# Kernel tuning notes

Hardware: AMD Instinct MI355X
Metric: run time of the kernel (lower is better)

Reference implementation:

```python
import jax, jax.numpy as jnp
import numpy as np

NUM_HEADS = 16
HIDDEN = 64  # per-head dim


def setup_inputs() -> dict:
    key = jax.random.key(0)
    ks = jax.random.split(key, 7)
    B, Nq, S, D = 2, 2048, 2048, 1024
    return {
        "queries": jax.random.normal(ks[0], (B, Nq, D), jnp.float32),
        "keys": jax.random.normal(ks[1], (B, S, D), jnp.float32),
        "values": jax.random.normal(ks[2], (B, S, D), jnp.float32),
        "Wq": jax.random.normal(ks[3], (D, NUM_HEADS * HIDDEN), jnp.float32) * 0.02,
        "Wk": jax.random.normal(ks[4], (D, NUM_HEADS * HIDDEN), jnp.float32) * 0.02,
        "Wv": jax.random.normal(ks[5], (D, NUM_HEADS * HIDDEN), jnp.float32) * 0.02,
        "Wo": jax.random.normal(ks[6], (NUM_HEADS * HIDDEN, 1024), jnp.float32) * 0.02,
    }


def reference(queries, keys, values, Wq, Wk, Wv, Wo):
    B, Nq, _ = queries.shape
    S = keys.shape[1]
    H, dh = NUM_HEADS, HIDDEN
    # projections, split heads: [B, len, H, dh] -> [B, H, len, dh]
    Q = (queries @ Wq).reshape(B, Nq, H, dh).transpose(0, 2, 1, 3)
    K = (keys @ Wk).reshape(B, S, H, dh).transpose(0, 2, 1, 3)
    V = (values @ Wv).reshape(B, S, H, dh).transpose(0, 2, 1, 3)
    scores = jnp.einsum("bhqd,bhkd->bhqk", Q, K) / jnp.sqrt(jnp.float32(dh))
    # NOTE: faithful to original -- softmax over ALL keys, THEN multiply by
    # strictly-lower-triangular mask (triangular * (1 - diagonal)); no renorm.
    P = jax.nn.softmax(scores, axis=-1)
    mask = jnp.tril(jnp.ones((Nq, S), jnp.float32), -1)  # strict lower triangle
    Sout = jnp.einsum("bhqk,bhkd->bhqd", P * mask, V)
    merged = Sout.transpose(0, 2, 1, 3).reshape(B, Nq, H * dh)
    return merged @ Wo
```

## Files before the change

kernel.cpp:

```cpp
#include <hip/hip_runtime.h>
#include <hip/hip_bf16.h>
#include <stdint.h>


typedef __bf16 bf16x8 __attribute__((ext_vector_type(8)));
typedef float f32x4 __attribute__((ext_vector_type(4)));
typedef unsigned int u32x4 __attribute__((ext_vector_type(4)));

typedef const __attribute__((address_space(1))) void* gas_t;
typedef __attribute__((address_space(3))) void* las_t;

__device__ __forceinline__ unsigned short f2bf(float f) {
    unsigned int u = __float_as_uint(f);
    return (unsigned short)((u + 0x7FFFu + ((u >> 16) & 1u)) >> 16);
}

__device__ __forceinline__ float exp2_hw(float x) {
    float r;
    asm("v_exp_f32 %0, %1" : "=v"(r) : "v"(x));
    return r;
}

__global__ __launch_bounds__(256) void cast_qkv(
    const float* __restrict__ q, const float* __restrict__ k, const float* __restrict__ v,
    unsigned short* __restrict__ oq, unsigned short* __restrict__ ok, unsigned short* __restrict__ ov)
{
    const float* src = (blockIdx.z == 0) ? q : (blockIdx.z == 1) ? k : v;
    unsigned short* dst = (blockIdx.z == 0) ? oq : (blockIdx.z == 1) ? ok : ov;
    unsigned int i = blockIdx.x * 256u + threadIdx.x;
    float4 f = reinterpret_cast<const float4*>(src)[i];
    ushort4 o;
    o.x = f2bf(f.x); o.y = f2bf(f.y); o.z = f2bf(f.z); o.w = f2bf(f.w);
    reinterpret_cast<ushort4*>(dst)[i] = o;
}

__global__ __launch_bounds__(256) void transpose_w(
    const float* __restrict__ w0, const float* __restrict__ w1,
    const float* __restrict__ w2, const float* __restrict__ w3,
    unsigned short* __restrict__ t0, unsigned short* __restrict__ t1,
    unsigned short* __restrict__ t2, unsigned short* __restrict__ t3)
{
    const float* W = (blockIdx.z == 0) ? w0 : (blockIdx.z == 1) ? w1 : (blockIdx.z == 2) ? w2 : w3;
    unsigned short* T = (blockIdx.z == 0) ? t0 : (blockIdx.z == 1) ? t1 : (blockIdx.z == 2) ? t2 : t3;
    __shared__ float s[32][33];
    const int tx = threadIdx.x, ty = threadIdx.y;
    const int x = blockIdx.x * 32 + tx;
#pragma unroll
    for (int j = 0; j < 4; ++j)
        s[ty + 8 * j][tx] = W[(size_t)(blockIdx.y * 32 + ty + 8 * j) * 1024 + x];
    __syncthreads();
    const int xo = blockIdx.y * 32 + tx;
#pragma unroll
    for (int j = 0; j < 4; ++j)
        T[(size_t)(blockIdx.x * 32 + ty + 8 * j) * 1024 + xo] = f2bf(s[tx][ty + 8 * j]);
}

__global__ __launch_bounds__(256) void transpose_v(
    const unsigned short* __restrict__ Vp, unsigned short* __restrict__ Vt)
{
    __shared__ unsigned short s[64][68];
    const int tid = threadIdx.x;
    const int s0 = blockIdx.x * 64, h = blockIdx.y, b = blockIdx.z;
    const size_t inbase = ((size_t)(b * 2048 + s0)) * 1024 + h * 64;
#pragma unroll
    for (int r = 0; r < 4; ++r) {
        int idx = r * 256 + tid;
        int row = idx >> 4;
        int c4 = (idx & 15) * 4;
        ushort4 v = *(const ushort4*)(Vp + inbase + (size_t)row * 1024 + c4);
        *(ushort4*)&s[row][c4] = v;
    }
    __syncthreads();
    const size_t outbase = ((size_t)((b * 16 + h) * 64)) * 2048 + s0;
#pragma unroll
    for (int r = 0; r < 4; ++r) {
        int idx = r * 256 + tid;
        int drow = idx >> 4;
        int sc = (idx & 15) * 4;
        ushort4 v;
        v.x = s[sc][drow]; v.y = s[sc + 1][drow]; v.z = s[sc + 2][drow]; v.w = s[sc + 3][drow];
        *(ushort4*)(Vt + outbase + (size_t)drow * 2048 + sc) = v;
    }
}

template <int BM, int BN, int MODE>
__global__ __launch_bounds__(256) void gemm_bt(
    const unsigned short* __restrict__ A0, const unsigned short* __restrict__ A1,
    const unsigned short* __restrict__ A2,
    const unsigned short* __restrict__ B0, const unsigned short* __restrict__ B1,
    const unsigned short* __restrict__ B2,
    unsigned short* __restrict__ C0, unsigned short* __restrict__ C1,
    unsigned short* __restrict__ C2, float* __restrict__ Cf)
{
    constexpr int K = 1024;
    constexpr int WM = BM / 2, WN = BN / 2, MI = WM / 16, NI = WN / 16;
    __shared__ __align__(16) unsigned char lds[(BM + BN) * 64];
    unsigned char* lA = lds;
    unsigned char* lB = lds + BM * 64;

    const int tid = threadIdx.x;
    const int z = blockIdx.z;
    const unsigned short* A  = (MODE == 1 || z == 0) ? A0 : (z == 1) ? A1 : A2;
    const unsigned short* Bt = (MODE == 1 || z == 0) ? B0 : (z == 1) ? B1 : B2;
    const int m0 = blockIdx.y * BM, n0 = blockIdx.x * BN;
    const int w = tid >> 6, lane = tid & 63, g = lane >> 4, l15 = lane & 15;
    const int wr = w >> 1, wc = w & 1;

    f32x4 acc[MI][NI] = {};

    for (int k0 = 0; k0 < K; k0 += 32) {
#pragma unroll
        for (int r = 0; r < (BM * 64) / 4096; ++r) {
            const int o = (r * 256 + tid) * 16;
            const unsigned char* gp = (const unsigned char*)A
                + ((size_t)(m0 + (o >> 6)) * K + k0) * 2 + (o & 63);
            __builtin_amdgcn_global_load_lds((gas_t)gp,
                (las_t)(lA + (r * 256 + (tid & ~63)) * 16), 16, 0, 0);
        }
#pragma unroll
        for (int r = 0; r < (BN * 64) / 4096; ++r) {
            const int o = (r * 256 + tid) * 16;
            const unsigned char* gp = (const unsigned char*)Bt
                + ((size_t)(n0 + (o >> 6)) * K + k0) * 2 + (o & 63);
            __builtin_amdgcn_global_load_lds((gas_t)gp,
                (las_t)(lB + (r * 256 + (tid & ~63)) * 16), 16, 0, 0);
        }
        __syncthreads();

        bf16x8 a[MI], bfr[NI];
#pragma unroll
        for (int mi = 0; mi < MI; ++mi)
            a[mi] = *(const bf16x8*)(lA + (wr * WM + mi * 16 + l15) * 64 + g * 16);
#pragma unroll
        for (int ni = 0; ni < NI; ++ni)
            bfr[ni] = *(const bf16x8*)(lB + (wc * WN + ni * 16 + l15) * 64 + g * 16);
#pragma unroll
        for (int mi = 0; mi < MI; ++mi)
#pragma unroll
            for (int ni = 0; ni < NI; ++ni)
                acc[mi][ni] = __builtin_amdgcn_mfma_f32_16x16x32_bf16(a[mi], bfr[ni], acc[mi][ni], 0, 0, 0);
        __syncthreads();
    }

    if (MODE == 1) {
#pragma unroll
        for (int mi = 0; mi < MI; ++mi)
#pragma unroll
            for (int ni = 0; ni < NI; ++ni)
#pragma unroll
                for (int i = 0; i < 4; ++i) {
                    const int row = m0 + wr * WM + mi * 16 + 4 * g + i;
                    const int col = n0 + wc * WN + ni * 16 + l15;
                    Cf[(size_t)row * 1024 + col] = acc[mi][ni][i];
                }
    } else {
        unsigned short* C = (z == 0) ? C0 : (z == 1) ? C1 : C2;
        const float qscale = (z == 0) ? 0.18033688f : 1.0f;
#pragma unroll
        for (int mi = 0; mi < MI; ++mi)
#pragma unroll
            for (int ni = 0; ni < NI; ++ni)
#pragma unroll
                for (int i = 0; i < 4; ++i) {
                    const int row = m0 + wr * WM + mi * 16 + 4 * g + i;
                    const int col = n0 + wc * WN + ni * 16 + l15;
                    C[(size_t)row * 1024 + col] = f2bf(acc[mi][ni][i] * qscale);
                }
    }
}

__device__ __forceinline__ f32x4 qk_exp(const unsigned char* base, int rowoff,
                                        int ni, int g, int l15,
                                        bf16x8 aq0, bf16x8 aq1)
{
    const int row = rowoff + ni * 16 + l15;
    const int sw = (row & 7) << 4;
    const bf16x8 bk0 = *(const bf16x8*)(base + ((row * 128 + g * 16) ^ sw));
    const bf16x8 bk1 = *(const bf16x8*)(base + ((row * 128 + 64 + g * 16) ^ sw));
    f32x4 t = {};
    t = __builtin_amdgcn_mfma_f32_16x16x32_bf16(bk0, aq0, t, 0, 0, 0);
    t = __builtin_amdgcn_mfma_f32_16x16x32_bf16(bk1, aq1, t, 0, 0, 0);
    f32x4 r;
#pragma unroll
    for (int i = 0; i < 4; ++i) r[i] = exp2_hw(t[i]);
    return r;
}

__global__ __launch_bounds__(256) void attn_kernel(
    const unsigned short* __restrict__ Qp, const unsigned short* __restrict__ Kp,
    const unsigned short* __restrict__ Vt, unsigned short* __restrict__ mrg)
{
    __shared__ __align__(16) unsigned char lds[24576];
    __shared__ float dden[4][16];
    unsigned char* Ks = lds;
    unsigned char* Vs = lds + 8192;
    unsigned char* Ps = lds + 16384;

    const int tid = threadIdx.x;
    const int w = tid >> 6, lane = tid & 63, g = lane >> 4, l15 = lane & 15;
    const int bid = blockIdx.x;
    const int bh = (bid & 7) * 4 + ((bid >> 3) & 3);
    const int qt = 31 - (bid >> 5);
    const int b = bh >> 4, hd = bh & 15;
    const int q0 = qt * 64;

    bf16x8 aq0, aq1;
    {
        const unsigned short* qp = Qp + ((size_t)(b * 2048 + q0 + 16 * w + l15) * 1024 + hd * 64 + g * 8);
        aq0 = *(const bf16x8*)qp;
        aq1 = *(const bf16x8*)(qp + 32);
    }

    const unsigned char* Kbase = (const unsigned char*)Kp + ((size_t)(b * 2048) * 1024 + hd * 64) * 2;
    const unsigned char* Vbase = (const unsigned char*)Vt + ((size_t)bh * 64) * 2048 * 2;

    const int o0 = tid * 16,         r0 = o0 >> 7;
    const int o1 = (256 + tid) * 16, r1 = o1 >> 7;
    const int o2 = (512 + tid) * 16, r2 = o2 >> 7;
    const int o3 = (768 + tid) * 16, r3 = o3 >> 7;

    f32x4 oacc[4] = {};
    f32x4 dsum = {0.f, 0.f, 0.f, 0.f};

    const int prow = 16 * w + l15;
    const int pb   = prow * 128;
    const int psw  = l15 << 3;

    uint4 kr0, kr1, vr0, vr1, cr0, cr1, cr2, cr3;
    kr0 = *(const uint4*)(Kbase + (size_t)r0 * 2048 + (o0 & 127));
    kr1 = *(const uint4*)(Kbase + (size_t)r1 * 2048 + (o1 & 127));
    vr0 = *(const uint4*)(Vbase + (size_t)r0 * 4096 + (o0 & 127));
    vr1 = *(const uint4*)(Vbase + (size_t)r1 * 4096 + (o1 & 127));

    for (int t = 0; t <= qt; ++t) {
        __syncthreads();
        *(uint4*)(Ks + (o0 ^ ((r0 & 7) << 4))) = kr0;
        *(uint4*)(Ks + (o1 ^ ((r1 & 7) << 4))) = kr1;
        *(uint4*)(Vs + (o0 ^ ((r0 & 7) << 4))) = vr0;
        *(uint4*)(Vs + (o1 ^ ((r1 & 7) << 4))) = vr1;
        if (t < qt) {
            const int k1 = (t + 1) * 64;
            kr0 = *(const uint4*)(Kbase + (size_t)(k1 + r0) * 2048 + (o0 & 127));
            kr1 = *(const uint4*)(Kbase + (size_t)(k1 + r1) * 2048 + (o1 & 127));
            vr0 = *(const uint4*)(Vbase + (size_t)r0 * 4096 + (size_t)k1 * 2 + (o0 & 127));
            vr1 = *(const uint4*)(Vbase + (size_t)r1 * 4096 + (size_t)k1 * 2 + (o1 & 127));
        } else if (qt < 31) {
            const int kc = (qt + 1) * 64;
            const int nk = 2048 - kc;
            cr0 = *(const uint4*)(Kbase + (size_t)(kc + r0) * 2048 + (o0 & 127));
            cr1 = *(const uint4*)(Kbase + (size_t)(kc + r1) * 2048 + (o1 & 127));
            if (nk > 64) {
                cr2 = *(const uint4*)(Kbase + (size_t)(kc + r2) * 2048 + (o2 & 127));
                cr3 = *(const uint4*)(Kbase + (size_t)(kc + r3) * 2048 + (o3 & 127));
            }
        }
        __syncthreads();

        f32x4 pe[4];
#pragma unroll
        for (int ni = 0; ni < 4; ++ni) {
            pe[ni] = qk_exp(Ks, 0, ni, g, l15, aq0, aq1);
            dsum += pe[ni];
        }
        if (t == qt) {
#pragma unroll
            for (int ni = 0; ni < 4; ++ni)
#pragma unroll
                for (int i = 0; i < 4; ++i)
                    if (ni * 16 + 4 * g + i >= prow) pe[ni][i] = 0.f;
        }
#pragma unroll
        for (int ni = 0; ni < 4; ++ni) {
            unsigned int lo, hi;
            asm("v_cvt_pk_bf16_f32 %0, %1, %2" : "=v"(lo) : "v"(pe[ni][0]), "v"(pe[ni][1]));
            asm("v_cvt_pk_bf16_f32 %0, %1, %2" : "=v"(hi) : "v"(pe[ni][2]), "v"(pe[ni][3]));
            uint2 pv; pv.x = lo; pv.y = hi;
            *(uint2*)(Ps + ((pb + ni * 32 + g * 8) ^ psw)) = pv;
        }
#pragma unroll
        for (int kk = 0; kk < 2; ++kk) {
            const uint2 a0 = *(const uint2*)(Ps + ((pb + kk * 64 + g * 16) ^ psw));
            const uint2 a1 = *(const uint2*)(Ps + ((pb + kk * 64 + g * 16 + 8) ^ psw));
            u32x4 au; au.x = a0.x; au.y = a0.y; au.z = a1.x; au.w = a1.y;
            const bf16x8 pa = *(const bf16x8*)&au;
#pragma unroll
            for (int ni = 0; ni < 4; ++ni) {
                const int rv = ni * 16 + l15;
                const bf16x8 bv = *(const bf16x8*)(Vs + ((rv * 128 + kk * 64 + g * 16) ^ ((rv & 7) << 4)));
                oacc[ni] = __builtin_amdgcn_mfma_f32_16x16x32_bf16(pa, bv, oacc[ni], 0, 0, 0);
            }
        }
    }

    for (int kc = (qt + 1) * 64; kc < 2048; kc += 128) {
        const int nk = min(128, 2048 - kc);
        __syncthreads();
        *(uint4*)(lds + (o0 ^ ((r0 & 7) << 4))) = cr0;
        *(uint4*)(lds + (o1 ^ ((r1 & 7) << 4))) = cr1;
        if (nk > 64) {
            *(uint4*)(lds + (o2 ^ ((r2 & 7) << 4))) = cr2;
            *(uint4*)(lds + (o3 ^ ((r3 & 7) << 4))) = cr3;
        }
        const int kn = kc + 128;
        if (kn < 2048) {
            const int nk2 = 2048 - kn;
            cr0 = *(const uint4*)(Kbase + (size_t)(kn + r0) * 2048 + (o0 & 127));
            cr1 = *(const uint4*)(Kbase + (size_t)(kn + r1) * 2048 + (o1 & 127));
            if (nk2 > 64) {
                cr2 = *(const uint4*)(Kbase + (size_t)(kn + r2) * 2048 + (o2 & 127));
                cr3 = *(const uint4*)(Kbase + (size_t)(kn + r3) * 2048 + (o3 & 127));
            }
        }
        __syncthreads();
        for (int koff = 0; koff < nk; koff += 64)
#pragma unroll
            for (int ni = 0; ni < 4; ++ni)
                dsum += qk_exp(lds, koff, ni, g, l15, aq0, aq1);
    }

    float den = dsum[0] + dsum[1] + dsum[2] + dsum[3];
    den += __shfl_xor(den, 16, 64);
    den += __shfl_xor(den, 32, 64);
    if (lane < 16) dden[w][lane] = den;
    float inv[4];
#pragma unroll
    for (int i = 0; i < 4; ++i) inv[i] = 1.0f / dden[w][4 * g + i];
#pragma unroll
    for (int ni = 0; ni < 4; ++ni)
#pragma unroll
        for (int i = 0; i < 4; ++i) {
            const int row = q0 + 16 * w + 4 * g + i;
            mrg[((size_t)b * 2048 + row) * 1024 + hd * 64 + ni * 16 + l15] =
                f2bf(oacc[ni][i] * inv[i]);
        }
}

extern "C" void kernel_launch(void* const* d_in, const int* in_sizes, int n_in,
                              void* d_out, int out_size, void* d_ws, size_t ws_size,
                              hipStream_t stream)
{
    const float* q  = (const float*)d_in[0];
    const float* k  = (const float*)d_in[1];
    const float* v  = (const float*)d_in[2];
    const float* Wq = (const float*)d_in[3];
    const float* Wk = (const float*)d_in[4];
    const float* Wv = (const float*)d_in[5];
    const float* Wo = (const float*)d_in[6];
    float* out = (float*)d_out;

    unsigned short* ws = (unsigned short*)d_ws;
    const size_t TEN = (size_t)2 * 2048 * 1024;
    unsigned short* qbf = ws;
    unsigned short* kbf = ws + TEN;
    unsigned short* vbf = ws + 2 * TEN;
    unsigned short* Wqt = ws + 3 * TEN;
    unsigned short* Wkt = Wqt + 1024 * 1024;
    unsigned short* Wvt = Wkt + 1024 * 1024;
    unsigned short* Wot = Wvt + 1024 * 1024;
    unsigned short* Qp  = ws + 4 * TEN;
    unsigned short* Kp  = ws + 5 * TEN;
    unsigned short* Vp  = ws + 6 * TEN;
    unsigned short* Vt  = qbf;
    unsigned short* mrg = kbf;

    cast_qkv<<<dim3(4096, 1, 3), 256, 0, stream>>>(q, k, v, qbf, kbf, vbf);
    transpose_w<<<dim3(32, 32, 4), dim3(32, 8), 0, stream>>>(Wq, Wk, Wv, Wo, Wqt, Wkt, Wvt, Wot);
    gemm_bt<128, 128, 0><<<dim3(8, 32, 3), 256, 0, stream>>>(
        qbf, kbf, vbf, Wqt, Wkt, Wvt, Qp, Kp, Vp, nullptr);
    transpose_v<<<dim3(32, 16, 2), 256, 0, stream>>>(Vp, Vt);
    attn_kernel<<<dim3(1024, 1, 1), 256, 0, stream>>>(Qp, Kp, Vt, mrg);
    gemm_bt<64, 128, 1><<<dim3(8, 64, 1), 256, 0, stream>>>(
        mrg, nullptr, nullptr, Wot, nullptr, nullptr, nullptr, nullptr, nullptr, out);
}
```

Measured before the change: 228.3 us.

## Double-buffer K/V tiles in LDS and merge denominator loop into main loop

Replaces the two-phase loop (masked PV tiles, then a separate denominator-only pass over the remaining keys in 128-row chunks) with a single 32-iteration loop over 64-key tiles. K and V tiles are ping-ponged between two LDS buffers, which removes one __syncthreads per iteration. Tiles past the diagonal only compute exp sums and skip the V load and PV MFMAs. The trade-off is more LDS (about 40KB instead of 24KB), which may lower occupancy, and more barriers in the tail phase, since it now walks 64-key tiles instead of 128.

```diff
diff --git a/kernel.cpp b/kernel.cpp
--- a/kernel.cpp
+++ b/kernel.cpp
@@ -169,11 +169,11 @@
     }
 }
 
-__device__ __forceinline__ f32x4 qk_exp(const unsigned char* base, int rowoff,
+__device__ __forceinline__ f32x4 qk_exp(const unsigned char* base,
                                         int ni, int g, int l15,
                                         bf16x8 aq0, bf16x8 aq1)
 {
-    const int row = rowoff + ni * 16 + l15;
+    const int row = ni * 16 + l15;
     const int sw = (row & 7) << 4;
     const bf16x8 bk0 = *(const bf16x8*)(base + ((row * 128 + g * 16) ^ sw));
     const bf16x8 bk1 = *(const bf16x8*)(base + ((row * 128 + 64 + g * 16) ^ sw));
@@ -190,11 +190,10 @@
     const unsigned short* __restrict__ Qp, const unsigned short* __restrict__ Kp,
     const unsigned short* __restrict__ Vt, unsigned short* __restrict__ mrg)
 {
-    __shared__ __align__(16) unsigned char lds[24576];
+    __shared__ __align__(16) unsigned char Kb[16384];
+    __shared__ __align__(16) unsigned char Vb[16384];
+    __shared__ __align__(16) unsigned char Ps[8192];
     __shared__ float dden[4][16];
-    unsigned char* Ks = lds;
-    unsigned char* Vs = lds + 8192;
-    unsigned char* Ps = lds + 16384;
 
     const int tid = threadIdx.x;
     const int w = tid >> 6, lane = tid & 63, g = lane >> 4, l15 = lane & 15;
@@ -216,8 +215,8 @@
 
     const int o0 = tid * 16,         r0 = o0 >> 7;
     const int o1 = (256 + tid) * 16, r1 = o1 >> 7;
-    const int o2 = (512 + tid) * 16, r2 = o2 >> 7;
-    const int o3 = (768 + tid) * 16, r3 = o3 >> 7;
+    const int so0 = o0 ^ ((r0 & 7) << 4);
+    const int so1 = o1 ^ ((r1 & 7) << 4);
 
     f32x4 oacc[4] = {};
     f32x4 dsum = {0.f, 0.f, 0.f, 0.f};
@@ -226,32 +225,28 @@
     const int pb   = prow * 128;
     const int psw  = l15 << 3;
 
-    uint4 kr0, kr1, vr0, vr1, cr0, cr1, cr2, cr3;
+    uint4 kr0, kr1, vr0, vr1;
     kr0 = *(const uint4*)(Kbase + (size_t)r0 * 2048 + (o0 & 127));
     kr1 = *(const uint4*)(Kbase + (size_t)r1 * 2048 + (o1 & 127));
     vr0 = *(const uint4*)(Vbase + (size_t)r0 * 4096 + (o0 & 127));
     vr1 = *(const uint4*)(Vbase + (size_t)r1 * 4096 + (o1 & 127));
 
-    for (int t = 0; t <= qt; ++t) {
-        __syncthreads();
-        *(uint4*)(Ks + (o0 ^ ((r0 & 7) << 4))) = kr0;
-        *(uint4*)(Ks + (o1 ^ ((r1 & 7) << 4))) = kr1;
-        *(uint4*)(Vs + (o0 ^ ((r0 & 7) << 4))) = vr0;
-        *(uint4*)(Vs + (o1 ^ ((r1 & 7) << 4))) = vr1;
-        if (t < qt) {
+    for (int t = 0; t < 32; ++t) {
+        unsigned char* Ks = Kb + (t & 1) * 8192;
+        unsigned char* Vs = Vb + (t & 1) * 8192;
+        *(uint4*)(Ks + so0) = kr0;
+        *(uint4*)(Ks + so1) = kr1;
+        if (t <= qt) {
+            *(uint4*)(Vs + so0) = vr0;
+            *(uint4*)(Vs + so1) = vr1;
+        }
+        if (t < 31) {
             const int k1 = (t + 1) * 64;
             kr0 = *(const uint4*)(Kbase + (size_t)(k1 + r0) * 2048 + (o0 & 127));
             kr1 = *(const uint4*)(Kbase + (size_t)(k1 + r1) * 2048 + (o1 & 127));
-            vr0 = *(const uint4*)(Vbase + (size_t)r0 * 4096 + (size_t)k1 * 2 + (o0 & 127));
-            vr1 = *(const uint4*)(Vbase + (size_t)r1 * 4096 + (size_t)k1 * 2 + (o1 & 127));
-        } else if (qt < 31) {
-            const int kc = (qt + 1) * 64;
-            const int nk = 2048 - kc;
-            cr0 = *(const uint4*)(Kbase + (size_t)(kc + r0) * 2048 + (o0 & 127));
-            cr1 = *(const uint4*)(Kbase + (size_t)(kc + r1) * 2048 + (o1 & 127));
-            if (nk > 64) {
-                cr2 = *(const uint4*)(Kbase + (size_t)(kc + r2) * 2048 + (o2 & 127));
-                cr3 = *(const uint4*)(Kbase + (size_t)(kc + r3) * 2048 + (o3 & 127));
+            if (t + 1 <= qt) {
+                vr0 = *(const uint4*)(Vbase + (size_t)r0 * 4096 + (size_t)k1 * 2 + (o0 & 127));
+                vr1 = *(const uint4*)(Vbase + (size_t)r1 * 4096 + (size_t)k1 * 2 + (o1 & 127));
             }
         }
         __syncthreads();
@@ -259,9 +254,11 @@
         f32x4 pe[4];
 #pragma unroll
         for (int ni = 0; ni < 4; ++ni) {
-            pe[ni] = qk_exp(Ks, 0, ni, g, l15, aq0, aq1);
+            pe[ni] = qk_exp(Ks, ni, g, l15, aq0, aq1);
             dsum += pe[ni];
         }
+        if (t > qt) continue;
+
         if (t == qt) {
 #pragma unroll
             for (int ni = 0; ni < 4; ++ni)
@@ -290,32 +287,6 @@
                 oacc[ni] = __builtin_amdgcn_mfma_f32_16x16x32_bf16(pa, bv, oacc[ni], 0, 0, 0);
             }
         }
-    }
-
-    for (int kc = (qt + 1) * 64; kc < 2048; kc += 128) {
-        const int nk = min(128, 2048 - kc);
-        __syncthreads();
-        *(uint4*)(lds + (o0 ^ ((r0 & 7) << 4))) = cr0;
-        *(uint4*)(lds + (o1 ^ ((r1 & 7) << 4))) = cr1;
-        if (nk > 64) {
-            *(uint4*)(lds + (o2 ^ ((r2 & 7) << 4))) = cr2;
-            *(uint4*)(lds + (o3 ^ ((r3 & 7) << 4))) = cr3;
-        }
-        const int kn = kc + 128;
-        if (kn < 2048) {
-            const int nk2 = 2048 - kn;
-            cr0 = *(const uint4*)(Kbase + (size_t)(kn + r0) * 2048 + (o0 & 127));
-            cr1 = *(const uint4*)(Kbase + (size_t)(kn + r1) * 2048 + (o1 & 127));
-            if (nk2 > 64) {
-                cr2 = *(const uint4*)(Kbase + (size_t)(kn + r2) * 2048 + (o2 & 127));
-                cr3 = *(const uint4*)(Kbase + (size_t)(kn + r3) * 2048 + (o3 & 127));
-            }
-        }
-        __syncthreads();
-        for (int koff = 0; koff < nk; koff += 64)
-#pragma unroll
-            for (int ni = 0; ni < 4; ++ni)
-                dsum += qk_exp(lds, koff, ni, g, l15, aq0, aq1);
     }
 
     float den = dsum[0] + dsum[1] + dsum[2] + dsum[3];
```

After: 229.4 us. Within noise of the previous version (+0.5%).
